# Kernel optimization log

Hardware: AMD Instinct MI355X
Metric: run time of the kernel (lower is better)

## Reference

```python
import jax, jax.numpy as jnp
import numpy as np

EPS = 1e-5
NUM_HEADS = 4
HEAD_DIM = 64
NUM_STEPS = 3


def layernorm(x, g, b):
    mu = jnp.mean(x, axis=-1, keepdims=True)
    var = jnp.mean((x - mu) ** 2, axis=-1, keepdims=True)
    return (x - mu) / jnp.sqrt(var + EPS) * g + b


def entmax15(x):
    # exact alpha=1.5 entmax along last axis (Peters et al. 2019)
    n = x.shape[-1]
    x = x - jnp.max(x, axis=-1, keepdims=True)
    x = x / 2.0
    srt = -jnp.sort(-x, axis=-1)                      # descending
    rho = jnp.arange(1, n + 1, dtype=x.dtype)
    cs = jnp.cumsum(srt, axis=-1)
    cs2 = jnp.cumsum(srt * srt, axis=-1)
    mean = cs / rho
    ss = cs2 - mean * cs                              # k * (mean_sq - mean^2)
    delta = (1.0 - ss) / rho
    d = jnp.clip(delta, 0.0)
    safe = jnp.where(d > 0, d, 1.0)
    tau = mean - jnp.where(d > 0, jnp.sqrt(safe), 0.0)
    support = (tau <= srt).astype(jnp.int32)
    k_star = jnp.sum(support, axis=-1, keepdims=True) - 1
    tau_star = jnp.take_along_axis(tau, k_star, axis=-1)
    p = jnp.clip(x - tau_star, 0.0)
    return p * p


def setup_inputs() -> dict:
    key = jax.random.key(0)
    ks = jax.random.split(key, 8)
    B, S, Dh = 2, 512, 2048
    N, Dm = 8192, 1024
    T = NUM_HEADS * HEAD_DIM  # 256
    hidden = jax.random.normal(ks[0], (B, S, Dh), dtype=jnp.float32)
    memory = jax.random.normal(ks[1], (N, Dm), dtype=jnp.float32)
    Wq = jax.random.normal(ks[2], (Dh, T), dtype=jnp.float32) * 0.02
    Wk = jax.random.normal(ks[3], (Dm, T), dtype=jnp.float32) * 0.02
    Wv = jax.random.normal(ks[4], (Dm, T), dtype=jnp.float32) * 0.02
    Wo = jax.random.normal(ks[5], (T, Dh), dtype=jnp.float32) * 0.02
    log_beta = jnp.full((NUM_HEADS,), float(np.log(1.0 / np.sqrt(HEAD_DIM))), dtype=jnp.float32)
    g_s = jnp.ones((Dh,), jnp.float32)
    b_s = jnp.zeros((Dh,), jnp.float32)
    g_m = jnp.ones((Dm,), jnp.float32)
    b_m = jnp.zeros((Dm,), jnp.float32)
    return {"hidden": hidden, "memory": memory, "Wq": Wq, "Wk": Wk, "Wv": Wv,
            "Wo": Wo, "log_beta": log_beta, "g_s": g_s, "b_s": b_s,
            "g_m": g_m, "b_m": b_m}


def reference(hidden, memory, Wq, Wk, Wv, Wo, log_beta, g_s, b_s, g_m, b_m):
    B, S, _ = hidden.shape
    N = memory.shape[0]
    H, D = NUM_HEADS, HEAD_DIM
    Q = layernorm(hidden, g_s, b_s) @ Wq                         # [B,S,H*D]
    mem_n = layernorm(memory, g_m, b_m)
    K = (mem_n @ Wk).reshape(N, H, D).transpose(1, 0, 2)         # [H,N,D]
    V = (mem_n @ Wv).reshape(N, H, D).transpose(1, 0, 2)         # [H,N,D]
    xi = Q.reshape(B, S, H, D).transpose(0, 2, 1, 3)             # [B,H,S,D]
    beta = jnp.exp(log_beta)[None, :, None, None]                # [1,H,1,1]
    for _ in range(NUM_STEPS):
        scores = jnp.einsum('bhsd,hnd->bhsn', xi, K) * beta      # [B,H,S,N]
        w = entmax15(scores)
        xi = jnp.einsum('bhsn,hnd->bhsd', w, V)
    converged = xi.transpose(0, 2, 1, 3).reshape(B, S, H * D)
    output = converged @ Wo                                      # [B,S,hidden_dim]
    return output, converged
```

## Files before the change

### kernel.cpp

```cpp
#include <hip/hip_runtime.h>
#include <math.h>

typedef _Float16 f16;
typedef f16 f16x8 __attribute__((ext_vector_type(8)));
typedef float f32x4 __attribute__((ext_vector_type(4)));

#define QSCALE 16384.0f
#define QINV 6.103515625e-5f
#define QOFF 2.5f

__device__ __forceinline__ float wred_add(float v) {
#pragma unroll
  for (int off = 32; off >= 1; off >>= 1) v += __shfl_xor(v, off, 64);
  return v;
}
__device__ __forceinline__ float wred_max(float v) {
#pragma unroll
  for (int off = 32; off >= 1; off >>= 1) v = fmaxf(v, __shfl_xor(v, off, 64));
  return v;
}

__global__ __launch_bounds__(256) void ln_stats_kernel(
    const float* __restrict__ X, int cols, float* __restrict__ mu,
    float* __restrict__ rs) {
  int row = blockIdx.x, tid = threadIdx.x;
  const float4* xr = (const float4*)(X + (size_t)row * cols);
  int nv = cols >> 10;
  float s = 0.f, s2 = 0.f;
  for (int v = 0; v < nv; ++v) {
    float4 x4 = xr[tid + (v << 8)];
    s += x4.x + x4.y + x4.z + x4.w;
    s2 += x4.x * x4.x + x4.y * x4.y + x4.z * x4.z + x4.w * x4.w;
  }
  s = wred_add(s);
  s2 = wred_add(s2);
  __shared__ float rb[8];
  int wid = tid >> 6, lane = tid & 63;
  if (lane == 0) { rb[wid] = s; rb[4 + wid] = s2; }
  __syncthreads();
  if (tid == 0) {
    float S = rb[0] + rb[1] + rb[2] + rb[3];
    float S2 = rb[4] + rb[5] + rb[6] + rb[7];
    float m = S / (float)cols;
    float var = S2 / (float)cols - m * m;
    mu[row] = m;
    rs[row] = 1.f / sqrtf(var + 1e-5f);
  }
}

__global__ __launch_bounds__(256) void split_a_kernel(
    const float* __restrict__ X, const float* __restrict__ mu,
    const float* __restrict__ rs, f16x8* __restrict__ Ah,
    f16x8* __restrict__ Al, int M, int Kd, int lay) {
  int blk = blockIdx.x * 4 + (threadIdx.x >> 6);
  int l = threadIdx.x & 63;
  int nmt = M >> 4;
  int kc = blk / nmt, mt = blk - kc * nmt;
  int m = mt * 16 + (l & 15);
  int k = kc * 32 + ((l >> 4) << 3);
  const float* src;
  if (lay == 0) {
    src = X + (size_t)m * Kd + k;
  } else {
    int b = m >> 9, s = m & 511, hh = k >> 6, d = k & 63;
    src = X + ((((size_t)b * 4 + hh) * 512 + s) << 6) + d;
  }
  float mm = mu ? mu[m] : 0.f;
  float rr = rs ? rs[m] : 1.f;
  f16x8 hi, lo;
#pragma unroll
  for (int j = 0; j < 8; ++j) {
    float v = (src[j] - mm) * rr;
    f16 hv = (f16)v;
    hi[j] = hv;
    lo[j] = (f16)((v - (float)hv) * 512.f);
  }
  size_t o = ((size_t)blk << 6) + l;
  Ah[o] = hi;
  Al[o] = lo;
}

__global__ __launch_bounds__(256) void split_w_kernel(
    const float* __restrict__ W, const float* __restrict__ g,
    f16x8* __restrict__ Bh, f16x8* __restrict__ Bl, int Kd, int N) {
  int blk = blockIdx.x * 4 + (threadIdx.x >> 6);
  int l = threadIdx.x & 63;
  int nnt = N >> 4;
  int kc = blk / nnt, nt = blk - kc * nnt;
  int n = nt * 16 + (l & 15);
  int k0 = kc * 32 + ((l >> 4) << 3);
  f16x8 hi, lo;
#pragma unroll
  for (int j = 0; j < 8; ++j) {
    float v = W[(size_t)(k0 + j) * N + n];
    if (g) v *= g[k0 + j];
    f16 hv = (f16)v;
    hi[j] = hv;
    lo[j] = (f16)((v - (float)hv) * 512.f);
  }
  size_t o = ((size_t)blk << 6) + l;
  Bh[o] = hi;
  Bl[o] = lo;
}

__global__ __launch_bounds__(256) void wcol_kernel(
    const float* __restrict__ W, const float* __restrict__ b,
    float* __restrict__ vb, int Kd, int N) {
  int t = blockIdx.x * 256 + threadIdx.x;
  int kpb = Kd >> 4;
  int k0 = blockIdx.y * kpb;
  float s = 0.f;
  for (int k = k0; k < k0 + kpb; ++k) s = fmaf(b[k], W[(size_t)k * N + t], s);
  atomicAdd(&vb[t], s);
}

__global__ __launch_bounds__(256) void gemm_mfma_kernel(
    const f16x8* __restrict__ Ah, const f16x8* __restrict__ Al,
    const f16x8* __restrict__ Bh, const f16x8* __restrict__ Bl,
    const float* __restrict__ vb, float* __restrict__ outf,
    f16x8* __restrict__ o16a, f16x8* __restrict__ o16b, int M, int N, int nk,
    int out_mode) {
  __shared__ __align__(16) float Ts[64][68];
  const int tid = threadIdx.x;
  const int w = tid >> 6, l = tid & 63;
  const int ql = l & 15, g = l >> 4;
  const int bn = blockIdx.x, bm = blockIdx.y;
  const size_t astr = ((size_t)(M >> 4)) << 6;
  const size_t bstr = ((size_t)(N >> 4)) << 6;
  const f16x8* aph = Ah + (((size_t)(bm * 4 + w)) << 6) + l;
  const f16x8* apl = Al + (((size_t)(bm * 4 + w)) << 6) + l;
  const f16x8* bph = Bh + (((size_t)(bn * 4)) << 6) + l;
  const f16x8* bpl = Bl + (((size_t)(bn * 4)) << 6) + l;

  f32x4 cm[4], cx[4];
#pragma unroll
  for (int nf = 0; nf < 4; ++nf) {
    cm[nf] = (f32x4){0.f, 0.f, 0.f, 0.f};
    cx[nf] = (f32x4){0.f, 0.f, 0.f, 0.f};
  }

  f16x8 a0h = aph[0], a0l = apl[0];
  f16x8 b0h[4], b0l[4];
#pragma unroll
  for (int nf = 0; nf < 4; ++nf) {
    b0h[nf] = bph[nf << 6];
    b0l[nf] = bpl[nf << 6];
  }

  for (int kc = 0; kc < nk - 1; ++kc) {
    const size_t ao = (size_t)(kc + 1) * astr;
    const size_t bo = (size_t)(kc + 1) * bstr;
    f16x8 a1h = aph[ao], a1l = apl[ao];
    f16x8 b1h[4], b1l[4];
#pragma unroll
    for (int nf = 0; nf < 4; ++nf) {
      b1h[nf] = bph[bo + (nf << 6)];
      b1l[nf] = bpl[bo + (nf << 6)];
    }
#pragma unroll
    for (int nf = 0; nf < 4; ++nf) {
      cm[nf] = __builtin_amdgcn_mfma_f32_16x16x32_f16(a0h, b0h[nf], cm[nf], 0, 0, 0);
      cx[nf] = __builtin_amdgcn_mfma_f32_16x16x32_f16(a0h, b0l[nf], cx[nf], 0, 0, 0);
      cx[nf] = __builtin_amdgcn_mfma_f32_16x16x32_f16(a0l, b0h[nf], cx[nf], 0, 0, 0);
    }
    a0h = a1h;
    a0l = a1l;
#pragma unroll
    for (int nf = 0; nf < 4; ++nf) {
      b0h[nf] = b1h[nf];
      b0l[nf] = b1l[nf];
    }
  }
#pragma unroll
  for (int nf = 0; nf < 4; ++nf) {
    cm[nf] = __builtin_amdgcn_mfma_f32_16x16x32_f16(a0h, b0h[nf], cm[nf], 0, 0, 0);
    cx[nf] = __builtin_amdgcn_mfma_f32_16x16x32_f16(a0h, b0l[nf], cx[nf], 0, 0, 0);
    cx[nf] = __builtin_amdgcn_mfma_f32_16x16x32_f16(a0l, b0h[nf], cx[nf], 0, 0, 0);
  }

  float vbc[4] = {0.f, 0.f, 0.f, 0.f};
  if (vb) {
#pragma unroll
    for (int nf = 0; nf < 4; ++nf) vbc[nf] = vb[bn * 64 + nf * 16 + ql];
  }

  if (out_mode == 0) {
#pragma unroll
    for (int nf = 0; nf < 4; ++nf)
#pragma unroll
      for (int r = 0; r < 4; ++r) {
        float val = fmaf(cx[nf][r], 0.001953125f, cm[nf][r]) + vbc[nf];
        int m = bm * 64 + w * 16 + (g << 2) + r;
        int n = bn * 64 + nf * 16 + ql;
        int b = m >> 9, s = m & 511, hh = n >> 6, d = n & 63;
        outf[((((size_t)b * 4 + hh) * 512 + s) << 6) + d] = val;
      }
  } else if (out_mode == 3) {
#pragma unroll
    for (int nf = 0; nf < 4; ++nf)
#pragma unroll
      for (int r = 0; r < 4; ++r) {
        float val = fmaf(cx[nf][r], 0.001953125f, cm[nf][r]) + vbc[nf];
        int m = bm * 64 + w * 16 + (g << 2) + r;
        int n = bn * 64 + nf * 16 + ql;
        outf[(size_t)m * N + n] = val;
      }
  } else {
#pragma unroll
    for (int nf = 0; nf < 4; ++nf)
#pragma unroll
      for (int r = 0; r < 4; ++r)
        Ts[w * 16 + (g << 2) + r][nf * 16 + ql] =
            fmaf(cx[nf][r], 0.001953125f, cm[nf][r]) + vbc[nf];
    __syncthreads();
    if (out_mode == 4) {
#pragma unroll
      for (int i = 0; i < 2; ++i) {
        int slot = tid + (i << 8);
        int blk = slot >> 6, l2 = slot & 63;
        int ktl = blk >> 1, dc = blk & 1;
        int key = (ktl << 4) + (l2 & 15);
        int db = (dc << 5) + ((l2 >> 4) << 3);
        f16x8 hi, lo;
#pragma unroll
        for (int j = 0; j < 8; ++j) {
          float v = Ts[key][db + j];
          f16 hv = (f16)v;
          hi[j] = hv;
          lo[j] = (f16)((v - (float)hv) * 512.f);
        }
        size_t o = (((size_t)(bn * 512 + bm * 4 + ktl) * 2 + dc) << 6) + l2;
        o16a[o] = hi;
        o16b[o] = lo;
      }
    } else {
#pragma unroll
      for (int i = 0; i < 2; ++i) {
        int slot = tid + (i << 8);
        int blk = slot >> 6, l2 = slot & 63;
        int dt = blk >> 1, kcl = blk & 1;
        int keyb = (kcl << 5) + ((l2 >> 4) << 3);
        int d = (dt << 4) + (l2 & 15);
        f16x8 v8;
#pragma unroll
        for (int j = 0; j < 8; ++j) v8[j] = (f16)Ts[keyb + j][d];
        size_t o = (((size_t)(bn * 4 + dt) * 256 + bm * 2 + kcl) << 6) + l2;
        o16a[o] = v8;
      }
    }
  }
}

__global__ __launch_bounds__(512) void hop_score_kernel(
    const float* __restrict__ xi_in, const f16x8* __restrict__ Khi,
    const f16x8* __restrict__ Klo, const float* __restrict__ log_beta,
    unsigned short* __restrict__ Y) {
  __shared__ float xiq[16][64];
  __shared__ float mxb[8][16];
  __shared__ float mxs[16];
  const int tid = threadIdx.x;
  const int w = tid >> 6, l = tid & 63;
  const int ql = l & 15, g = l >> 4;
  const int bh = blockIdx.x & 7, qtile = blockIdx.x >> 3;
  const int h = bh & 3;
  const size_t base_io = ((size_t)bh * 512 + qtile * 16) * 64;

  float beta = expf(log_beta[h]);
  for (int i = tid; i < 1024; i += 512)
    xiq[i >> 6][i & 63] = xi_in[base_io + i] * beta;
  __syncthreads();

  f16x8 xh0, xh1, xl0, xl1;
#pragma unroll
  for (int j = 0; j < 8; ++j) {
    float x0 = xiq[ql][(g << 3) + j];
    float x1 = xiq[ql][32 + (g << 3) + j];
    f16 h0 = (f16)x0, h1 = (f16)x1;
    xh0[j] = h0; xl0[j] = (f16)((x0 - (float)h0) * 512.f);
    xh1[j] = h1; xl1[j] = (f16)((x1 - (float)h1) * 512.f);
  }

  const f16x8* kb = Khi + (size_t)h * 65536 + l;
  const f16x8* kl = Klo + (size_t)h * 65536 + l;
  const int kt0 = w * 64;

  float mymax = -3.4e38f;
  for (int kt = kt0; kt < kt0 + 8; ++kt) {
    f32x4 c = {0.f, 0.f, 0.f, 0.f};
    c = __builtin_amdgcn_mfma_f32_16x16x32_f16(kb[(size_t)kt * 128], xh0, c, 0, 0, 0);
    c = __builtin_amdgcn_mfma_f32_16x16x32_f16(kb[(size_t)kt * 128 + 64], xh1, c, 0, 0, 0);
    mymax = fmaxf(fmaxf(fmaxf(c[0], c[1]), fmaxf(c[2], c[3])), mymax);
  }
  mymax = fmaxf(mymax, __shfl_xor(mymax, 16, 64));
  mymax = fmaxf(mymax, __shfl_xor(mymax, 32, 64));
  if (l < 16) mxb[w][ql] = mymax;
  __syncthreads();
  if (tid < 16) {
    float m = mxb[0][tid];
#pragma unroll
    for (int ww = 1; ww < 8; ++ww) m = fmaxf(m, mxb[ww][tid]);
    mxs[tid] = m;
  }
  __syncthreads();
  const float mh = mxs[ql] * 0.5f;

  const size_t Ybase = (size_t)(bh * 32 + qtile) * 131072;
  for (int kt = kt0; kt < kt0 + 64; ++kt) {
    f16x8 a0 = kb[(size_t)kt * 128], a1 = kb[(size_t)kt * 128 + 64];
    f16x8 b0 = kl[(size_t)kt * 128], b1 = kl[(size_t)kt * 128 + 64];
    f32x4 cm = {0.f, 0.f, 0.f, 0.f}, cx = {0.f, 0.f, 0.f, 0.f};
    cm = __builtin_amdgcn_mfma_f32_16x16x32_f16(a0, xh0, cm, 0, 0, 0);
    cm = __builtin_amdgcn_mfma_f32_16x16x32_f16(a1, xh1, cm, 0, 0, 0);
    cx = __builtin_amdgcn_mfma_f32_16x16x32_f16(b0, xh0, cx, 0, 0, 0);
    cx = __builtin_amdgcn_mfma_f32_16x16x32_f16(a0, xl0, cx, 0, 0, 0);
    cx = __builtin_amdgcn_mfma_f32_16x16x32_f16(b1, xh1, cx, 0, 0, 0);
    cx = __builtin_amdgcn_mfma_f32_16x16x32_f16(a1, xl1, cx, 0, 0, 0);
    ushort4 uv;
    unsigned short* up = (unsigned short*)&uv;
#pragma unroll
    for (int r = 0; r < 4; ++r) {
      float s = fmaf(cx[r], 0.001953125f, cm[r]);
      float y = fmaf(s, 0.5f, -mh);
      float uq = fmaf(y, QSCALE, QOFF * QSCALE + 0.5f);
      uq = fminf(fmaxf(uq, 0.f), 65535.f);
      up[r] = (unsigned short)(int)uq;
    }
    *(ushort4*)&Y[Ybase + (size_t)(kt >> 1) * 512 + ql * 32 + (kt & 1) * 16 +
                  (g << 2)] = uv;
  }
}

__global__ __launch_bounds__(256) void hop_tau_kernel(
    const unsigned short* __restrict__ Y, float* __restrict__ tau) {
  const int row = blockIdx.x;
  const int bh = row >> 9, qi = row & 511;
  const int qtile = qi >> 4, ql = qi & 15;
  const size_t yb = (size_t)(bh * 32 + qtile) * 131072 + ql * 32;
  const int t = threadIdx.x;
  const uint4* p = (const uint4*)(Y + yb + (size_t)t * 512);
  float y[32];
#pragma unroll
  for (int v = 0; v < 4; ++v) {
    uint4 u = p[v];
    unsigned a[4] = {u.x, u.y, u.z, u.w};
#pragma unroll
    for (int e = 0; e < 4; ++e) {
      y[v * 8 + e * 2] = fmaf((float)(a[e] & 0xffffu), QINV, -QOFF);
      y[v * 8 + e * 2 + 1] = fmaf((float)(a[e] >> 16), QINV, -QOFF);
    }
  }
  __shared__ float rb[4];
  __shared__ float rb3[4][3];
  float lo = -1.1f, hi = 0.1f;
  const int wi = t >> 6, lane = t & 63;
#pragma unroll 1
  for (int it = 0; it < 9; ++it) {
    float tv = 0.5f * (lo + hi);
    float f = 0.f;
#pragma unroll
    for (int i = 0; i < 32; ++i) {
      float d = fmaxf(y[i] - tv, 0.f);
      f = fmaf(d, d, f);
    }
    f = wred_add(f);
    if (lane == 0) rb[wi] = f;
    __syncthreads();
    float tot = rb[0] + rb[1] + rb[2] + rb[3];
    if (tot >= 1.f) lo = tv; else hi = tv;
    __syncthreads();
  }
  float tc = lo;
#pragma unroll 1
  for (int it = 0; it < 2; ++it) {
    float kk = 0.f, s1 = 0.f, s2 = 0.f;
#pragma unroll
    for (int i = 0; i < 32; ++i) {
      if (y[i] > tc) { kk += 1.f; s1 += y[i]; s2 = fmaf(y[i], y[i], s2); }
    }
    kk = wred_add(kk);
    s1 = wred_add(s1);
    s2 = wred_add(s2);
    if (lane == 0) { rb3[wi][0] = kk; rb3[wi][1] = s1; rb3[wi][2] = s2; }
    __syncthreads();
    float K = rb3[0][0] + rb3[1][0] + rb3[2][0] + rb3[3][0];
    float S1 = rb3[0][1] + rb3[1][1] + rb3[2][1] + rb3[3][1];
    float S2 = rb3[0][2] + rb3[1][2] + rb3[2][2] + rb3[3][2];
    __syncthreads();
    if (K >= 0.5f) {
      float mean = S1 / K;
      float ss = fmaf(-mean, S1, S2);
      float delta = (1.f - ss) / K;
      tc = delta > 0.f ? mean - sqrtf(delta) : mean;
    }
  }
  if (t == 0) tau[row] = tc;
}

__global__ __launch_bounds__(512) void hop_pv_kernel(
    const unsigned short* __restrict__ Y, const f16x8* __restrict__ Vp,
    const float* __restrict__ tau, float* __restrict__ xi_out) {
  __shared__ float outp[8][16][64];
  __shared__ float taus[16];
  const int tid = threadIdx.x;
  const int w = tid >> 6, l = tid & 63;
  const int ql = l & 15, g = l >> 4;
  const int bh = blockIdx.x & 7, qtile = blockIdx.x >> 3;
  const int h = bh & 3;
  const size_t base_io = ((size_t)bh * 512 + qtile * 16) * 64;

  if (tid < 16) taus[tid] = tau[bh * 512 + qtile * 16 + tid];
  __syncthreads();
  const float t1 = taus[ql];
  const size_t Ybase = (size_t)(bh * 32 + qtile) * 131072;
  const f16x8* vb = Vp + (size_t)h * 65536 + l;

  f32x4 m2[4];
#pragma unroll
  for (int dt = 0; dt < 4; ++dt) m2[dt] = (f32x4){0.f, 0.f, 0.f, 0.f};

  for (int kc = 0; kc < 32; ++kc) {
    const int chunk = w * 32 + kc;
    uint4 uv = *(const uint4*)(Y + Ybase + (size_t)chunk * 512 + ql * 32 +
                               (g << 3));
    unsigned a[4] = {uv.x, uv.y, uv.z, uv.w};
    f16x8 a2;
#pragma unroll
    for (int e = 0; e < 4; ++e) {
      float y0 = fmaf((float)(a[e] & 0xffffu), QINV, -QOFF);
      float y1 = fmaf((float)(a[e] >> 16), QINV, -QOFF);
      float p0 = fmaxf(y0 - t1, 0.f);
      float p1 = fmaxf(y1 - t1, 0.f);
      a2[e * 2] = (f16)(p0 * p0);
      a2[e * 2 + 1] = (f16)(p1 * p1);
    }
#pragma unroll
    for (int dt = 0; dt < 4; ++dt) {
      f16x8 vf = vb[(((size_t)dt * 256 + chunk) << 6)];
      m2[dt] = __builtin_amdgcn_mfma_f32_16x16x32_f16(a2, vf, m2[dt], 0, 0, 0);
    }
  }
#pragma unroll
  for (int dt = 0; dt < 4; ++dt)
#pragma unroll
    for (int r = 0; r < 4; ++r)
      outp[w][(g << 2) + r][dt * 16 + ql] = m2[dt][r];
  __syncthreads();
  for (int i = tid; i < 1024; i += 512) {
    float s = 0.f;
#pragma unroll
    for (int ww = 0; ww < 8; ++ww) s += outp[ww][i >> 6][i & 63];
    xi_out[base_io + i] = s;
  }
}

__global__ __launch_bounds__(256) void conv_copy_kernel(
    const float* __restrict__ xi, float* __restrict__ out) {
  int o4 = blockIdx.x * 256 + threadIdx.x;
  int o = o4 << 2;
  int dd = o & 63, hq = (o >> 6) & 3, sq = (o >> 8) & 511, bq = o >> 17;
  float4 v =
      *(const float4*)&xi[((((size_t)bq << 2) + hq) * 512 + sq) * 64 + dd];
  *(float4*)&out[o] = v;
}

extern "C" void kernel_launch(void* const* d_in, const int* in_sizes, int n_in,
                              void* d_out, int out_size, void* d_ws,
                              size_t ws_size, hipStream_t stream) {
  (void)in_sizes; (void)n_in; (void)out_size; (void)ws_size;
  const float* hidden = (const float*)d_in[0];
  const float* memory = (const float*)d_in[1];
  const float* Wq = (const float*)d_in[2];
  const float* Wk = (const float*)d_in[3];
  const float* Wv = (const float*)d_in[4];
  const float* Wo = (const float*)d_in[5];
  const float* log_beta = (const float*)d_in[6];
  const float* g_s = (const float*)d_in[7];
  const float* b_s = (const float*)d_in[8];
  const float* g_m = (const float*)d_in[9];
  const float* b_m = (const float*)d_in[10];
  float* out = (float*)d_out;

  float* ws = (float*)d_ws;
  float* mu_h = ws;
  float* rs_h = ws + 1024;
  float* mu_m = ws + 2048;
  float* rs_m = ws + 10240;
  float* xiA = ws + 18432;
  float* xiB = ws + 280576;
  float* vb_q = ws + 542720;
  float* vb_k = ws + 542976;
  float* vb_v = ws + 543232;
  float* tau = ws + 543488;
  f16x8* Khi = (f16x8*)(ws + 548864);
  f16x8* Klo = Khi + 262144;
  f16x8* Vp = Klo + 262144;
  f16x8* Bqh = Vp + 262144;
  f16x8* Bql = Bqh + 65536;
  f16x8* Bkh = Bql + 65536;
  f16x8* Bkl = Bkh + 32768;
  f16x8* Bvh = Bkl + 32768;
  f16x8* Bvl = Bvh + 32768;
  f16x8* Boh = Bvl + 32768;
  f16x8* Bol = Boh + 65536;
  unsigned short* Y = (unsigned short*)(Bol + 65536);
  f16x8* Amh = (f16x8*)Y;
  f16x8* Aml = Amh + 1048576;
  f16x8* Ahh = Aml + 1048576;
  f16x8* Ahl = Ahh + 262144;
  f16x8* Axh = Ahl + 262144;
  f16x8* Axl = Axh + 32768;

  ln_stats_kernel<<<1024, 256, 0, stream>>>(hidden, 2048, mu_h, rs_h);
  ln_stats_kernel<<<8192, 256, 0, stream>>>(memory, 1024, mu_m, rs_m);
  hipMemsetAsync(vb_q, 0, 3 * 256 * sizeof(float), stream);

  split_a_kernel<<<1024, 256, 0, stream>>>(hidden, mu_h, rs_h, Ahh, Ahl, 1024,
                                           2048, 0);
  split_a_kernel<<<4096, 256, 0, stream>>>(memory, mu_m, rs_m, Amh, Aml, 8192,
                                           1024, 0);
  split_w_kernel<<<256, 256, 0, stream>>>(Wq, g_s, Bqh, Bql, 2048, 256);
  split_w_kernel<<<128, 256, 0, stream>>>(Wk, g_m, Bkh, Bkl, 1024, 256);
  split_w_kernel<<<128, 256, 0, stream>>>(Wv, g_m, Bvh, Bvl, 1024, 256);
  split_w_kernel<<<256, 256, 0, stream>>>(Wo, nullptr, Boh, Bol, 256, 2048);
  wcol_kernel<<<dim3(1, 16), 256, 0, stream>>>(Wq, b_s, vb_q, 2048, 256);
  wcol_kernel<<<dim3(1, 16), 256, 0, stream>>>(Wk, b_m, vb_k, 1024, 256);
  wcol_kernel<<<dim3(1, 16), 256, 0, stream>>>(Wv, b_m, vb_v, 1024, 256);

  gemm_mfma_kernel<<<dim3(4, 16), 256, 0, stream>>>(
      Ahh, Ahl, Bqh, Bql, vb_q, xiA, nullptr, nullptr, 1024, 256, 64, 0);
  gemm_mfma_kernel<<<dim3(4, 128), 256, 0, stream>>>(
      Amh, Aml, Bkh, Bkl, vb_k, nullptr, Khi, Klo, 8192, 256, 32, 4);
  gemm_mfma_kernel<<<dim3(4, 128), 256, 0, stream>>>(
      Amh, Aml, Bvh, Bvl, vb_v, nullptr, Vp, nullptr, 8192, 256, 32, 5);

  float* xin = xiA;
  float* xout = xiB;
  for (int step = 0; step < 3; ++step) {
    hop_score_kernel<<<256, 512, 0, stream>>>(xin, Khi, Klo, log_beta, Y);
    hop_tau_kernel<<<4096, 256, 0, stream>>>(Y, tau);
    hop_pv_kernel<<<256, 512, 0, stream>>>(Y, Vp, tau, xout);
    float* t = xin; xin = xout; xout = t;
  }

  split_a_kernel<<<128, 256, 0, stream>>>(xin, nullptr, nullptr, Axh, Axl,
                                          1024, 256, 1);
  gemm_mfma_kernel<<<dim3(32, 16), 256, 0, stream>>>(
      Axh, Axl, Boh, Bol, nullptr, out, nullptr, nullptr, 1024, 2048, 8, 3);
  conv_copy_kernel<<<256, 256, 0, stream>>>(xin, out + 2097152);
}
```

Baseline: 499.0 us.

## Trim entmax bisection, sample fewer tiles for max, fuse wcol launches

After: 462.6 us. 7.3% less time.

```diff
diff --git a/kernel.cpp b/kernel.cpp
--- a/kernel.cpp
+++ b/kernel.cpp
@@ -103,14 +103,22 @@
   Bl[o] = lo;
 }
 
-__global__ __launch_bounds__(256) void wcol_kernel(
-    const float* __restrict__ W, const float* __restrict__ b,
-    float* __restrict__ vb, int Kd, int N) {
-  int t = blockIdx.x * 256 + threadIdx.x;
+__global__ __launch_bounds__(256) void wcol3_kernel(
+    const float* __restrict__ Wq, const float* __restrict__ bq,
+    const float* __restrict__ Wk, const float* __restrict__ bk,
+    const float* __restrict__ Wv, const float* __restrict__ bv,
+    float* __restrict__ vbq, float* __restrict__ vbk,
+    float* __restrict__ vbv) {
+  int which = blockIdx.z;
+  const float* W = which == 0 ? Wq : (which == 1 ? Wk : Wv);
+  const float* b = which == 0 ? bq : (which == 1 ? bk : bv);
+  float* vb = which == 0 ? vbq : (which == 1 ? vbk : vbv);
+  int Kd = which == 0 ? 2048 : 1024;
+  int t = threadIdx.x;
   int kpb = Kd >> 4;
   int k0 = blockIdx.y * kpb;
   float s = 0.f;
-  for (int k = k0; k < k0 + kpb; ++k) s = fmaf(b[k], W[(size_t)k * N + t], s);
+  for (int k = k0; k < k0 + kpb; ++k) s = fmaf(b[k], W[(size_t)k * 256 + t], s);
   atomicAdd(&vb[t], s);
 }
 
@@ -285,7 +293,7 @@
   const int kt0 = w * 64;
 
   float mymax = -3.4e38f;
-  for (int kt = kt0; kt < kt0 + 8; ++kt) {
+  for (int kt = kt0; kt < kt0 + 2; ++kt) {
     f32x4 c = {0.f, 0.f, 0.f, 0.f};
     c = __builtin_amdgcn_mfma_f32_16x16x32_f16(kb[(size_t)kt * 128], xh0, c, 0, 0, 0);
     c = __builtin_amdgcn_mfma_f32_16x16x32_f16(kb[(size_t)kt * 128 + 64], xh1, c, 0, 0, 0);
@@ -303,6 +311,7 @@
   }
   __syncthreads();
   const float mh = mxs[ql] * 0.5f;
+  const float qc = QOFF * QSCALE + 0.5f - mh * QSCALE;
 
   const size_t Ybase = (size_t)(bh * 32 + qtile) * 131072;
   for (int kt = kt0; kt < kt0 + 64; ++kt) {
@@ -320,8 +329,7 @@
 #pragma unroll
     for (int r = 0; r < 4; ++r) {
       float s = fmaf(cx[r], 0.001953125f, cm[r]);
-      float y = fmaf(s, 0.5f, -mh);
-      float uq = fmaf(y, QSCALE, QOFF * QSCALE + 0.5f);
+      float uq = fmaf(s, 8192.0f, qc);
       uq = fminf(fmaxf(uq, 0.f), 65535.f);
       up[r] = (unsigned short)(int)uq;
     }
@@ -349,12 +357,25 @@
       y[v * 8 + e * 2 + 1] = fmaf((float)(a[e] >> 16), QINV, -QOFF);
     }
   }
-  __shared__ float rb[4];
-  __shared__ float rb3[4][3];
-  float lo = -1.1f, hi = 0.1f;
+  __shared__ float redm[4];
+  __shared__ float rb[5][4];
+  __shared__ float rb3[3][4][3];
   const int wi = t >> 6, lane = t & 63;
+
+  {
+    float m = y[0];
+#pragma unroll
+    for (int i = 1; i < 32; ++i) m = fmaxf(m, y[i]);
+    m = wred_max(m);
+    if (lane == 0) redm[wi] = m;
+  }
+  __syncthreads();
+  const float ymax =
+      fmaxf(fmaxf(redm[0], redm[1]), fmaxf(redm[2], redm[3]));
+
+  float lo = ymax - 1.001f, hi = ymax;
 #pragma unroll 1
-  for (int it = 0; it < 9; ++it) {
+  for (int it = 0; it < 5; ++it) {
     float tv = 0.5f * (lo + hi);
     float f = 0.f;
 #pragma unroll
@@ -363,15 +384,15 @@
       f = fmaf(d, d, f);
     }
     f = wred_add(f);
-    if (lane == 0) rb[wi] = f;
+    if (lane == 0) rb[it][wi] = f;
     __syncthreads();
-    float tot = rb[0] + rb[1] + rb[2] + rb[3];
+    float tot = rb[it][0] + rb[it][1] + rb[it][2] + rb[it][3];
     if (tot >= 1.f) lo = tv; else hi = tv;
-    __syncthreads();
-  }
+  }
+
   float tc = lo;
 #pragma unroll 1
-  for (int it = 0; it < 2; ++it) {
+  for (int it = 0; it < 3; ++it) {
     float kk = 0.f, s1 = 0.f, s2 = 0.f;
 #pragma unroll
     for (int i = 0; i < 32; ++i) {
@@ -380,12 +401,11 @@
     kk = wred_add(kk);
     s1 = wred_add(s1);
     s2 = wred_add(s2);
-    if (lane == 0) { rb3[wi][0] = kk; rb3[wi][1] = s1; rb3[wi][2] = s2; }
+    if (lane == 0) { rb3[it][wi][0] = kk; rb3[it][wi][1] = s1; rb3[it][wi][2] = s2; }
     __syncthreads();
-    float K = rb3[0][0] + rb3[1][0] + rb3[2][0] + rb3[3][0];
-    float S1 = rb3[0][1] + rb3[1][1] + rb3[2][1] + rb3[3][1];
-    float S2 = rb3[0][2] + rb3[1][2] + rb3[2][2] + rb3[3][2];
-    __syncthreads();
+    float K = rb3[it][0][0] + rb3[it][1][0] + rb3[it][2][0] + rb3[it][3][0];
+    float S1 = rb3[it][0][1] + rb3[it][1][1] + rb3[it][2][1] + rb3[it][3][1];
+    float S2 = rb3[it][0][2] + rb3[it][1][2] + rb3[it][2][2] + rb3[it][3][2];
     if (K >= 0.5f) {
       float mean = S1 / K;
       float ss = fmaf(-mean, S1, S2);
@@ -522,9 +542,8 @@
   split_w_kernel<<<128, 256, 0, stream>>>(Wk, g_m, Bkh, Bkl, 1024, 256);
   split_w_kernel<<<128, 256, 0, stream>>>(Wv, g_m, Bvh, Bvl, 1024, 256);
   split_w_kernel<<<256, 256, 0, stream>>>(Wo, nullptr, Boh, Bol, 256, 2048);
-  wcol_kernel<<<dim3(1, 16), 256, 0, stream>>>(Wq, b_s, vb_q, 2048, 256);
-  wcol_kernel<<<dim3(1, 16), 256, 0, stream>>>(Wk, b_m, vb_k, 1024, 256);
-  wcol_kernel<<<dim3(1, 16), 256, 0, stream>>>(Wv, b_m, vb_v, 1024, 256);
+  wcol3_kernel<<<dim3(1, 16, 3), 256, 0, stream>>>(Wq, b_s, Wk, b_m, Wv, b_m,
+                                                   vb_q, vb_k, vb_v);
 
   gemm_mfma_kernel<<<dim3(4, 16), 256, 0, stream>>>(
       Ahh, Ahl, Bqh, Bql, vb_q, xiA, nullptr, nullptr, 1024, 256, 64, 0);
```
